# Kernel optimization log

Hardware: AMD Instinct MI355X
Metric: run time of the kernel (lower is better)

## Reference

```python
import jax, jax.numpy as jnp
import numpy as np

N_NODES = 100000
N_EDGES = 1000000
M_DIM = 4
HID = 64
N_GRAPHS = 64


def setup_inputs() -> dict:
    key = jax.random.key(0)
    ks = jax.random.split(key, 16)
    x = jax.random.normal(ks[0], (N_NODES, 1, M_DIM), dtype=jnp.float32)
    edge_index = jax.random.randint(ks[1], (2, N_EDGES), 0, N_NODES, dtype=jnp.int64)
    batch = jnp.sort(jax.random.randint(ks[2], (N_NODES,), 0, N_GRAPHS, dtype=jnp.int64))
    def lin(k, out_c, in_c):
        bound = 1.0 / np.sqrt(in_c)
        return jax.random.uniform(k, (out_c, in_c), jnp.float32, -bound, bound)
    inp = {"x": x, "edge_index": edge_index, "batch": batch}
    inp["W1l"] = lin(ks[3], HID, 1); inp["b1l"] = jnp.zeros((HID,), jnp.float32)
    inp["W1r"] = lin(ks[4], HID, 1)
    inp["W2l"] = lin(ks[5], HID, HID); inp["b2l"] = jnp.zeros((HID,), jnp.float32)
    inp["W2r"] = lin(ks[6], HID, HID)
    inp["W3l"] = lin(ks[7], HID, HID); inp["b3l"] = jnp.zeros((HID,), jnp.float32)
    inp["W3r"] = lin(ks[8], HID, HID)
    inp["Wlin"] = lin(ks[9], 1, HID); inp["blin"] = jnp.zeros((1,), jnp.float32)
    return inp


def _sage_conv(x, src, dst, Wl, bl, Wr):
    # x: [N, F, M]; mean aggregation over in-edges, then lin_l/lin_r GEMMs.
    N, F, M = x.shape
    msg = x[src]  # [E, F, M] gather
    s = jax.ops.segment_sum(msg, dst, num_segments=N)
    cnt = jax.ops.segment_sum(jnp.ones((src.shape[0],), x.dtype), dst, num_segments=N)
    agg = s / jnp.maximum(cnt, 1.0)[:, None, None]  # [N, F, M]
    C = Wl.shape[0]
    # torch .view(N*M, F) on contiguous [N,F,M] == row-major reshape (mixes F and M)
    h = (agg.reshape(N * M, F) @ Wl.T + bl).reshape(N, C, M)
    h = h + (x.reshape(N * M, F) @ Wr.T).reshape(N, C, M)
    return h


def reference(x, edge_index, batch, W1l, b1l, W1r, W2l, b2l, W2r, W3l, b3l, W3r, Wlin, blin):
    src, dst = edge_index[0], edge_index[1]
    h = jax.nn.relu(_sage_conv(x, src, dst, W1l, b1l, W1r))
    h = jax.nn.relu(_sage_conv(h, src, dst, W2l, b2l, W2r))
    h = jax.nn.relu(_sage_conv(h, src, dst, W3l, b3l, W3r))
    # new_global_mean_pool: scatter-mean over nodes -> [B, HID, M]
    sums = jax.ops.segment_sum(h, batch, num_segments=N_GRAPHS)
    cnts = jax.ops.segment_sum(jnp.ones((h.shape[0],), h.dtype), batch, num_segments=N_GRAPHS)
    pooled = sums / jnp.maximum(cnts, 1.0)[:, None, None]
    # dropout in eval mode == identity
    B, F, M = pooled.shape
    z = (pooled.reshape(B * M, F) @ Wlin.T + blin).reshape(B, M)
    return jax.nn.sigmoid(z).mean(axis=1)  # [B]
```

## Files before the change

### kernel.cpp

```cpp
#include <hip/hip_runtime.h>
#include <math.h>

#define TPB 256

typedef unsigned short ushort_t;
typedef unsigned char uchar_t;
typedef __attribute__((ext_vector_type(8))) short short8v;
typedef __attribute__((ext_vector_type(4))) float f32x4;
typedef __attribute__((ext_vector_type(8))) unsigned short ushort8;

__device__ __forceinline__ unsigned short f2b(float f) {
  union { float f; unsigned int i; } c; c.f = f;
  unsigned int x = c.i;
  x += 0x7FFFu + ((x >> 16) & 1u);
  return (unsigned short)(x >> 16);
}

__device__ __forceinline__ short8v fp8x8_to_bf16(const uchar_t* p) {
  uint2 u = *(const uint2*)p;
  auto p0 = __builtin_amdgcn_cvt_pk_f32_fp8(u.x, false);
  auto p1 = __builtin_amdgcn_cvt_pk_f32_fp8(u.x, true);
  auto p2 = __builtin_amdgcn_cvt_pk_f32_fp8(u.y, false);
  auto p3 = __builtin_amdgcn_cvt_pk_f32_fp8(u.y, true);
  ushort8 o;
  o[0] = f2b(p0[0]); o[1] = f2b(p0[1]); o[2] = f2b(p1[0]); o[3] = f2b(p1[1]);
  o[4] = f2b(p2[0]); o[5] = f2b(p2[1]); o[6] = f2b(p3[0]); o[7] = f2b(p3[1]);
  union { ushort8 a; short8v b; } c; c.a = o; return c.b;
}

__global__ void k_histg(const int* __restrict__ dst, int* deg,
                        const int* __restrict__ batch, int* gcnt, int E, int N) {
  int t = blockIdx.x * TPB + threadIdx.x;
  if (t < E) atomicAdd(&deg[dst[t]], 1);
  int n0 = t * 16;
  if (n0 < N) {
    int n1 = min(n0 + 16, N);
    int cur = batch[n0];
    int c = 0;
    for (int n = n0; n < n1; ++n) {
      int b = batch[n];
      if (b != cur) { atomicAdd(&gcnt[cur], c); cur = b; c = 0; }
      ++c;
    }
    atomicAdd(&gcnt[cur], c);
  }
}

__global__ void k_scan1(const int* __restrict__ deg, int* rp, int* bsum, int N) {
  __shared__ int s[TPB];
  int t = threadIdx.x;
  int i = blockIdx.x * TPB + t;
  int v = (i < N) ? ((deg[i] + 7) & ~7) : 0;
  s[t] = v;
  __syncthreads();
  for (int d = 1; d < TPB; d <<= 1) {
    int u = (t >= d) ? s[t - d] : 0;
    __syncthreads();
    s[t] += u;
    __syncthreads();
  }
  if (i < N) rp[i] = s[t] - v;
  if (t == TPB - 1) bsum[blockIdx.x] = s[t];
}

__global__ void k_scan2(const int* bsum, int* boff, int nb) {
  __shared__ int s[1024];
  int t = threadIdx.x;
  int v = (t < nb) ? bsum[t] : 0;
  s[t] = v;
  __syncthreads();
  for (int d = 1; d < 1024; d <<= 1) {
    int u = (t >= d) ? s[t - d] : 0;
    __syncthreads();
    s[t] += u;
    __syncthreads();
  }
  if (t < nb) boff[t] = s[t] - v;
}

__global__ void k_scan3(int* rp, const int* __restrict__ boff, const int* __restrict__ bsum,
                        int* cursor, int N, int nb) {
  int i = blockIdx.x * TPB + threadIdx.x;
  if (i < N) {
    int v = rp[i] + boff[i >> 8];
    rp[i] = v;
    cursor[i] = v;
  } else if (i == N) {
    rp[N] = boff[nb - 1] + bsum[nb - 1];
  }
}

__global__ void k_fill(const int* __restrict__ src, const int* __restrict__ dst,
                       int* cursor, int* __restrict__ csr, int E) {
  int e = blockIdx.x * TPB + threadIdx.x;
  if (e < E) {
    int p = atomicAdd(&cursor[dst[e]], 1);
    csr[p] = src[e];
  }
}

__global__ void k_cvtw(const float* __restrict__ s0, const float* __restrict__ s1,
                       const float* __restrict__ s2, const float* __restrict__ s3,
                       ushort_t* d0, ushort_t* d1, ushort_t* d2, ushort_t* d3,
                       uchar_t* zr0, int n) {
  int i = blockIdx.x * TPB + threadIdx.x;
  if (i < n) { d0[i] = f2b(s0[i]); d1[i] = f2b(s1[i]); d2[i] = f2b(s2[i]); d3[i] = f2b(s3[i]); }
  if (blockIdx.x == 0 && threadIdx.x < 64) ((int*)zr0)[threadIdx.x] = 0;
}

__global__ void k_agg1(const float4* __restrict__ x, const int* __restrict__ rp,
                       const int* __restrict__ deg, const int* __restrict__ cursor,
                       int* __restrict__ csr, float4* __restrict__ agg1, int N) {
  int n = blockIdx.x * TPB + threadIdx.x;
  if (n >= N) return;
  int b = rp[n], e = rp[n + 1];
  float4 a = make_float4(0.f, 0.f, 0.f, 0.f);
  for (int i = b; i < e; i += 8) {
    int4 c0 = *(const int4*)(csr + i);
    int4 c1 = *(const int4*)(csr + i + 4);
    int id[8] = {c0.x, c0.y, c0.z, c0.w, c1.x, c1.y, c1.z, c1.w};
#pragma unroll
    for (int j = 0; j < 8; ++j) {
      unsigned idx = min((unsigned)id[j], (unsigned)(N - 1));
      float m = ((unsigned)id[j] < (unsigned)N) ? 1.f : 0.f;
      float4 v = x[idx];
      a.x += v.x * m; a.y += v.y * m; a.z += v.z * m; a.w += v.w * m;
    }
  }
  int d = deg[n];
  float inv = (d > 0) ? 1.f / (float)d : 0.f;
  a.x *= inv; a.y *= inv; a.z *= inv; a.w *= inv;
  agg1[n] = a;
  int c = cursor[n];
  for (int p2 = c; p2 < e; ++p2) csr[p2] = N;
}

__global__ __launch_bounds__(256) void k_gemm(
    const uchar_t* __restrict__ hIn8,
    const float* __restrict__ xf, const float* __restrict__ agg1f,
    const float* __restrict__ W1l, const float* __restrict__ b1l,
    const float* __restrict__ W1r,
    const ushort_t* __restrict__ Wlb, const ushort_t* __restrict__ Wrb,
    const float* __restrict__ bias,
    uchar_t* __restrict__ Yl8, uchar_t* __restrict__ Yr8, int rows) {
  int t = threadIdx.x;
  int wave = t >> 6, lane = t & 63;
  int g = lane >> 4, l15 = lane & 15;
  int r0 = blockIdx.x * 64 + wave * 16;
  int r = r0 + l15;

  short8v af0, af1;
  if (hIn8) {
    const uchar_t* hrow = hIn8 + (size_t)r * 64;
    af0 = fp8x8_to_bf16(hrow + g * 8);
    af1 = fp8x8_to_bf16(hrow + 32 + g * 8);
  } else {
    float sA = agg1f[r], sX = xf[r];
    ushort8 o0, o1;
#pragma unroll
    for (int k = 0; k < 8; ++k) {
      int c0 = g * 8 + k, c1 = 32 + g * 8 + k;
      o0[k] = f2b(fmaxf(sA * W1l[c0] + b1l[c0] + sX * W1r[c0], 0.f));
      o1[k] = f2b(fmaxf(sA * W1l[c1] + b1l[c1] + sX * W1r[c1], 0.f));
    }
    union { ushort8 a; short8v b; } u0, u1;
    u0.a = o0; u1.a = o1;
    af0 = u0.b; af1 = u1.b;
  }

#pragma unroll
  for (int c = 0; c < 4; ++c) {
    const ushort_t* wl = Wlb + (size_t)(c * 16 + l15) * 64;
    const ushort_t* wr = Wrb + (size_t)(c * 16 + l15) * 64;
    short8v bl0 = *(const short8v*)(wl + g * 8);
    short8v bl1 = *(const short8v*)(wl + 32 + g * 8);
    short8v br0 = *(const short8v*)(wr + g * 8);
    short8v br1 = *(const short8v*)(wr + 32 + g * 8);
    float bv = bias[c * 16 + l15];
    f32x4 accl = (f32x4){0.f, 0.f, 0.f, 0.f};
    f32x4 accr = (f32x4){bv, bv, bv, bv};
    accl = __builtin_amdgcn_mfma_f32_16x16x32_bf16(af0, bl0, accl, 0, 0, 0);
    accl = __builtin_amdgcn_mfma_f32_16x16x32_bf16(af1, bl1, accl, 0, 0, 0);
    accr = __builtin_amdgcn_mfma_f32_16x16x32_bf16(af0, br0, accr, 0, 0, 0);
    accr = __builtin_amdgcn_mfma_f32_16x16x32_bf16(af1, br1, accr, 0, 0, 0);
#pragma unroll
    for (int i = 0; i < 4; ++i) {
      size_t off = (size_t)(r0 + g * 4 + i) * 64 + c * 16 + l15;
      Yl8[off] = (uchar_t)(__builtin_amdgcn_cvt_pk_fp8_f32(accl[i], accl[i], 0u, false) & 0xFF);
      Yr8[off] = (uchar_t)(__builtin_amdgcn_cvt_pk_fp8_f32(accr[i], accr[i], 0u, false) & 0xFF);
    }
  }
}

#define ADD8(IDX) { \
    uint2 v = *(const uint2*)(base + ((size_t)(unsigned)(IDX) << 8)); \
    auto q0 = __builtin_amdgcn_cvt_pk_f32_fp8(v.x, false); \
    auto q1 = __builtin_amdgcn_cvt_pk_f32_fp8(v.x, true);  \
    auto q2 = __builtin_amdgcn_cvt_pk_f32_fp8(v.y, false); \
    auto q3 = __builtin_amdgcn_cvt_pk_f32_fp8(v.y, true);  \
    acc[0] += q0[0]; acc[1] += q0[1]; acc[2] += q1[0]; acc[3] += q1[1]; \
    acc[4] += q2[0]; acc[5] += q2[1]; acc[6] += q3[0]; acc[7] += q3[1]; }

__global__ __launch_bounds__(256) void k_gather(
    const uchar_t* __restrict__ Yl8, const uchar_t* __restrict__ Yr8,
    const int* __restrict__ rp, const int* __restrict__ deg, const int* __restrict__ csr,
    uchar_t* __restrict__ hOut8, int N) {
  int tid = blockIdx.x * TPB + threadIdx.x;
  int n = tid >> 5, s = tid & 31;
  if (n >= N) return;
  int b = rp[n], e = rp[n + 1];
  const uchar_t* base = Yl8 + s * 8;

  float acc[8];
#pragma unroll
  for (int j = 0; j < 8; ++j) acc[j] = 0.f;

  for (int i = b; i < e; i += 8) {
    int4 c0 = *(const int4*)(csr + i);
    int4 c1 = *(const int4*)(csr + i + 4);
    ADD8(c0.x) ADD8(c0.y) ADD8(c0.z) ADD8(c0.w)
    ADD8(c1.x) ADD8(c1.y) ADD8(c1.z) ADD8(c1.w)
  }

  int d = deg[n];
  float inv = (d > 0) ? 1.f / (float)d : 0.f;
  uint2 yr = *(const uint2*)(Yr8 + (size_t)n * 256 + s * 8);
  auto y0 = __builtin_amdgcn_cvt_pk_f32_fp8(yr.x, false);
  auto y1 = __builtin_amdgcn_cvt_pk_f32_fp8(yr.x, true);
  auto y2 = __builtin_amdgcn_cvt_pk_f32_fp8(yr.y, false);
  auto y3 = __builtin_amdgcn_cvt_pk_f32_fp8(yr.y, true);
  float h0 = fmaxf(acc[0] * inv + y0[0], 0.f);
  float h1 = fmaxf(acc[1] * inv + y0[1], 0.f);
  float h2 = fmaxf(acc[2] * inv + y1[0], 0.f);
  float h3 = fmaxf(acc[3] * inv + y1[1], 0.f);
  float h4 = fmaxf(acc[4] * inv + y2[0], 0.f);
  float h5 = fmaxf(acc[5] * inv + y2[1], 0.f);
  float h6 = fmaxf(acc[6] * inv + y3[0], 0.f);
  float h7 = fmaxf(acc[7] * inv + y3[1], 0.f);
  unsigned int w0 = __builtin_amdgcn_cvt_pk_fp8_f32(h0, h1, 0u, false);
  w0 = __builtin_amdgcn_cvt_pk_fp8_f32(h2, h3, w0, true);
  unsigned int w1 = __builtin_amdgcn_cvt_pk_fp8_f32(h4, h5, 0u, false);
  w1 = __builtin_amdgcn_cvt_pk_fp8_f32(h6, h7, w1, true);
  uint2 st; st.x = w0; st.y = w1;
  *(uint2*)(hOut8 + (size_t)n * 256 + s * 8) = st;
}

__device__ __forceinline__ float fp8_to_f32(uchar_t u) {
  return __builtin_amdgcn_cvt_pk_f32_fp8((unsigned int)u, false)[0];
}

__global__ void k_pool(const uchar_t* __restrict__ h, const int* __restrict__ batch,
                       float* pooled, int N) {
  int t = threadIdx.x;
  int nPer = (N + gridDim.x - 1) / gridDim.x;
  int n0 = blockIdx.x * nPer;
  int n1 = min(N, n0 + nPer);
  if (n0 >= n1) return;
  float acc = 0.f;
  int cur = batch[n0];
  int n = n0;
  for (; n + 3 < n1; n += 4) {
    int b0 = batch[n], b3 = batch[n + 3];
    float v0 = fp8_to_f32(h[(size_t)n * 256 + t]);
    float v1 = fp8_to_f32(h[(size_t)(n + 1) * 256 + t]);
    float v2 = fp8_to_f32(h[(size_t)(n + 2) * 256 + t]);
    float v3 = fp8_to_f32(h[(size_t)(n + 3) * 256 + t]);
    if (b0 == b3) {
      if (b0 != cur) { atomicAdd(&pooled[cur * 256 + t], acc); acc = 0.f; cur = b0; }
      acc += (v0 + v1) + (v2 + v3);
    } else {
      int bb1 = batch[n + 1], bb2 = batch[n + 2];
      int bb[4] = {b0, bb1, bb2, b3};
      float vv[4] = {v0, v1, v2, v3};
#pragma unroll
      for (int j = 0; j < 4; ++j) {
        if (bb[j] != cur) { atomicAdd(&pooled[cur * 256 + t], acc); acc = 0.f; cur = bb[j]; }
        acc += vv[j];
      }
    }
  }
  for (; n < n1; ++n) {
    int b = batch[n];
    if (b != cur) { atomicAdd(&pooled[cur * 256 + t], acc); acc = 0.f; cur = b; }
    acc += fp8_to_f32(h[(size_t)n * 256 + t]);
  }
  atomicAdd(&pooled[cur * 256 + t], acc);
}

__global__ void k_final(const float* __restrict__ pooled, const int* __restrict__ gcnt,
                        const float* __restrict__ Wlin, const float* __restrict__ blin,
                        float* __restrict__ out, int B) {
  int t = blockIdx.x * TPB + threadIdx.x;
  int b = t >> 2, j = t & 3;
  if (b >= B) return;
  float inv = 1.f / fmaxf((float)gcnt[b], 1.f);
  float s = blin[0];
  const float* p = pooled + b * 256 + j * 64;
#pragma unroll
  for (int f = 0; f < 64; ++f) s += p[f] * inv * Wlin[f];
  float z = 1.f / (1.f + expf(-s));
  z += __shfl_xor(z, 1);
  z += __shfl_xor(z, 2);
  if (j == 0) out[b] = 0.25f * z;
}

extern "C" void kernel_launch(void* const* d_in, const int* in_sizes, int n_in,
                              void* d_out, int out_size, void* d_ws, size_t ws_size,
                              hipStream_t stream) {
  const float* x   = (const float*)d_in[0];
  const int* edge  = (const int*)d_in[1];
  const int* batch = (const int*)d_in[2];
  const float* W1l = (const float*)d_in[3];
  const float* b1l = (const float*)d_in[4];
  const float* W1r = (const float*)d_in[5];
  const float* W2l = (const float*)d_in[6];
  const float* b2l = (const float*)d_in[7];
  const float* W2r = (const float*)d_in[8];
  const float* W3l = (const float*)d_in[9];
  const float* b3l = (const float*)d_in[10];
  const float* W3r = (const float*)d_in[11];
  const float* Wlin = (const float*)d_in[12];
  const float* blin = (const float*)d_in[13];
  float* out = (float*)d_out;

  const int N = in_sizes[0] / 4;
  const int E = in_sizes[1] / 2;
  const int B = out_size;
  const int rows = 4 * N;

  const int* srcA = edge;
  const int* dstA = edge + E;

  char* p = (char*)d_ws;
  auto carve = [&](size_t bytes) -> void* {
    void* r = (void*)p;
    p += (bytes + 255) & ~(size_t)255;
    return r;
  };
  char* zstart = p;
  int* deg     = (int*)carve((size_t)N * 4);
  int* gcnt    = (int*)carve((size_t)B * 4);
  float* pooled = (float*)carve((size_t)B * 256 * 4);
  size_t zlen  = (size_t)(p - zstart);
  int* rp      = (int*)carve((size_t)(N + 1) * 4);
  int* cursor  = (int*)carve((size_t)N * 4);
  int* bsum    = (int*)carve(4096);
  int* boff    = (int*)carve(4096);
  int* csr     = (int*)carve(((size_t)E + 8 * (size_t)N) * 4);
  float* agg1  = (float*)carve((size_t)N * 4 * 4);
  ushort_t* Wb2l = (ushort_t*)carve(4096 * 2);
  ushort_t* Wb2r = (ushort_t*)carve(4096 * 2);
  ushort_t* Wb3l = (ushort_t*)carve(4096 * 2);
  ushort_t* Wb3r = (ushort_t*)carve(4096 * 2);
  uchar_t* Yl8 = (uchar_t*)carve(((size_t)N + 1) * 256);
  uchar_t* Yr8 = (uchar_t*)carve((size_t)N * 256);
  uchar_t* h8  = (uchar_t*)carve((size_t)N * 256);
  (void)ws_size; (void)n_in;

  hipMemsetAsync(zstart, 0, zlen, stream);

  int nbScan = (N + TPB - 1) / TPB;

  k_histg<<<(E + TPB - 1) / TPB, TPB, 0, stream>>>(dstA, deg, batch, gcnt, E, N);
  k_cvtw<<<16, TPB, 0, stream>>>(W2l, W2r, W3l, W3r, Wb2l, Wb2r, Wb3l, Wb3r,
                                 Yl8 + (size_t)N * 256, 4096);
  k_scan1<<<nbScan, TPB, 0, stream>>>(deg, rp, bsum, N);
  k_scan2<<<1, 1024, 0, stream>>>(bsum, boff, nbScan);
  k_scan3<<<(N + 1 + TPB - 1) / TPB, TPB, 0, stream>>>(rp, boff, bsum, cursor, N, nbScan);
  k_fill<<<(E + TPB - 1) / TPB, TPB, 0, stream>>>(srcA, dstA, cursor, csr, E);

  k_agg1<<<(N + TPB - 1) / TPB, TPB, 0, stream>>>((const float4*)x, rp, deg, cursor,
                                                  csr, (float4*)agg1, N);

  int nbGemm = (rows + 63) / 64;
  int nbGather = ((size_t)N * 32 + TPB - 1) / TPB;

  k_gemm<<<nbGemm, TPB, 0, stream>>>((const uchar_t*)nullptr, x, agg1, W1l, b1l, W1r,
                                     Wb2l, Wb2r, b2l, Yl8, Yr8, rows);
  k_gather<<<nbGather, TPB, 0, stream>>>(Yl8, Yr8, rp, deg, csr, h8, N);

  k_gemm<<<nbGemm, TPB, 0, stream>>>(h8, x, agg1, W1l, b1l, W1r,
                                     Wb3l, Wb3r, b3l, Yl8, Yr8, rows);
  k_gather<<<nbGather, TPB, 0, stream>>>(Yl8, Yr8, rp, deg, csr, h8, N);

  k_pool<<<1024, TPB, 0, stream>>>(h8, batch, pooled, N);
  k_final<<<(B * 4 + TPB - 1) / TPB, TPB, 0, stream>>>(pooled, gcnt, Wlin, blin, out, B);
}
```

Baseline: 393.1 us.

## Bin edges by destination block for CSR fill and fuse pooling into final gather

The CSR fill becomes a two-pass binning. Edges are first scattered into coarse destination-block bins, and then each block places its bin's edges with atomics that stay local to that block, which should improve atomic and write locality. Separately, the last gather kernel now does the global mean-pool directly. It reduces across the block through shared memory when all 8 nodes belong to one graph and falls back to per-element atomics otherwise, so h8 is never written out and the separate pool kernel is gone. The cost is an extra pass over an 8-byte-per-edge bin buffer and more atomics in blocks that straddle a graph boundary.

```diff
diff --git a/kernel.cpp b/kernel.cpp
--- a/kernel.cpp
+++ b/kernel.cpp
@@ -90,12 +90,48 @@
   }
 }
 
-__global__ void k_fill(const int* __restrict__ src, const int* __restrict__ dst,
-                       int* cursor, int* __restrict__ csr, int E) {
+__global__ void k_bscan(const int* __restrict__ deg, int* bbase, int* bcur, int N, int nbk, int bshift) {
+  __shared__ int s[1024];
+  int t = threadIdx.x;
+  int cnt = 0;
+  if (t < nbk) {
+    int n0 = t << bshift, n1 = min(n0 + (1 << bshift), N);
+    for (int n = n0; n < n1; ++n) cnt += deg[n];
+  }
+  s[t] = cnt;
+  __syncthreads();
+  for (int d = 1; d < 1024; d <<= 1) {
+    int u = (t >= d) ? s[t - d] : 0;
+    __syncthreads();
+    s[t] += u;
+    __syncthreads();
+  }
+  if (t < nbk) {
+    int base = s[t] - cnt;
+    bbase[t] = base;
+    bcur[t] = base;
+    if (t == nbk - 1) bbase[nbk] = s[t];
+  }
+}
+
+__global__ void k_binA(const int* __restrict__ src, const int* __restrict__ dst,
+                       int* bcur, int2* __restrict__ binbuf, int E, int bshift) {
   int e = blockIdx.x * TPB + threadIdx.x;
   if (e < E) {
-    int p = atomicAdd(&cursor[dst[e]], 1);
-    csr[p] = src[e];
+    int d = dst[e], s = src[e];
+    int pos = atomicAdd(&bcur[d >> bshift], 1);
+    binbuf[pos] = make_int2(d, s);
+  }
+}
+
+__global__ void k_binB(const int2* __restrict__ binbuf, const int* __restrict__ bbase,
+                       int* cursor, int* __restrict__ csr) {
+  int b = blockIdx.x;
+  int lo = bbase[b], hi = bbase[b + 1];
+  for (int i = lo + threadIdx.x; i < hi; i += TPB) {
+    int2 pr = binbuf[i];
+    int p = atomicAdd(&cursor[pr.x], 1);
+    csr[p] = pr.y;
   }
 }
 
@@ -204,87 +240,85 @@
 __global__ __launch_bounds__(256) void k_gather(
     const uchar_t* __restrict__ Yl8, const uchar_t* __restrict__ Yr8,
     const int* __restrict__ rp, const int* __restrict__ deg, const int* __restrict__ csr,
-    uchar_t* __restrict__ hOut8, int N) {
+    uchar_t* __restrict__ hOut8, float* __restrict__ pooled,
+    const int* __restrict__ batch, int N) {
+  __shared__ float ps[1024];
   int tid = blockIdx.x * TPB + threadIdx.x;
   int n = tid >> 5, s = tid & 31;
-  if (n >= N) return;
-  int b = rp[n], e = rp[n + 1];
-  const uchar_t* base = Yl8 + s * 8;
+  bool alive = (n < N);
 
   float acc[8];
 #pragma unroll
   for (int j = 0; j < 8; ++j) acc[j] = 0.f;
 
-  for (int i = b; i < e; i += 8) {
-    int4 c0 = *(const int4*)(csr + i);
-    int4 c1 = *(const int4*)(csr + i + 4);
-    ADD8(c0.x) ADD8(c0.y) ADD8(c0.z) ADD8(c0.w)
-    ADD8(c1.x) ADD8(c1.y) ADD8(c1.z) ADD8(c1.w)
-  }
-
-  int d = deg[n];
-  float inv = (d > 0) ? 1.f / (float)d : 0.f;
-  uint2 yr = *(const uint2*)(Yr8 + (size_t)n * 256 + s * 8);
-  auto y0 = __builtin_amdgcn_cvt_pk_f32_fp8(yr.x, false);
-  auto y1 = __builtin_amdgcn_cvt_pk_f32_fp8(yr.x, true);
-  auto y2 = __builtin_amdgcn_cvt_pk_f32_fp8(yr.y, false);
-  auto y3 = __builtin_amdgcn_cvt_pk_f32_fp8(yr.y, true);
-  float h0 = fmaxf(acc[0] * inv + y0[0], 0.f);
-  float h1 = fmaxf(acc[1] * inv + y0[1], 0.f);
-  float h2 = fmaxf(acc[2] * inv + y1[0], 0.f);
-  float h3 = fmaxf(acc[3] * inv + y1[1], 0.f);
-  float h4 = fmaxf(acc[4] * inv + y2[0], 0.f);
-  float h5 = fmaxf(acc[5] * inv + y2[1], 0.f);
-  float h6 = fmaxf(acc[6] * inv + y3[0], 0.f);
-  float h7 = fmaxf(acc[7] * inv + y3[1], 0.f);
-  unsigned int w0 = __builtin_amdgcn_cvt_pk_fp8_f32(h0, h1, 0u, false);
-  w0 = __builtin_amdgcn_cvt_pk_fp8_f32(h2, h3, w0, true);
-  unsigned int w1 = __builtin_amdgcn_cvt_pk_fp8_f32(h4, h5, 0u, false);
-  w1 = __builtin_amdgcn_cvt_pk_fp8_f32(h6, h7, w1, true);
-  uint2 st; st.x = w0; st.y = w1;
-  *(uint2*)(hOut8 + (size_t)n * 256 + s * 8) = st;
-}
-
-__device__ __forceinline__ float fp8_to_f32(uchar_t u) {
-  return __builtin_amdgcn_cvt_pk_f32_fp8((unsigned int)u, false)[0];
-}
-
-__global__ void k_pool(const uchar_t* __restrict__ h, const int* __restrict__ batch,
-                       float* pooled, int N) {
-  int t = threadIdx.x;
-  int nPer = (N + gridDim.x - 1) / gridDim.x;
-  int n0 = blockIdx.x * nPer;
-  int n1 = min(N, n0 + nPer);
-  if (n0 >= n1) return;
-  float acc = 0.f;
-  int cur = batch[n0];
-  int n = n0;
-  for (; n + 3 < n1; n += 4) {
-    int b0 = batch[n], b3 = batch[n + 3];
-    float v0 = fp8_to_f32(h[(size_t)n * 256 + t]);
-    float v1 = fp8_to_f32(h[(size_t)(n + 1) * 256 + t]);
-    float v2 = fp8_to_f32(h[(size_t)(n + 2) * 256 + t]);
-    float v3 = fp8_to_f32(h[(size_t)(n + 3) * 256 + t]);
-    if (b0 == b3) {
-      if (b0 != cur) { atomicAdd(&pooled[cur * 256 + t], acc); acc = 0.f; cur = b0; }
-      acc += (v0 + v1) + (v2 + v3);
-    } else {
-      int bb1 = batch[n + 1], bb2 = batch[n + 2];
-      int bb[4] = {b0, bb1, bb2, b3};
-      float vv[4] = {v0, v1, v2, v3};
-#pragma unroll
-      for (int j = 0; j < 4; ++j) {
-        if (bb[j] != cur) { atomicAdd(&pooled[cur * 256 + t], acc); acc = 0.f; cur = bb[j]; }
-        acc += vv[j];
-      }
-    }
-  }
-  for (; n < n1; ++n) {
-    int b = batch[n];
-    if (b != cur) { atomicAdd(&pooled[cur * 256 + t], acc); acc = 0.f; cur = b; }
-    acc += fp8_to_f32(h[(size_t)n * 256 + t]);
-  }
-  atomicAdd(&pooled[cur * 256 + t], acc);
+  float h[8];
+#pragma unroll
+  for (int j = 0; j < 8; ++j) h[j] = 0.f;
+
+  if (alive) {
+    int b = rp[n], e = rp[n + 1];
+    const uchar_t* base = Yl8 + s * 8;
+    for (int i = b; i < e; i += 8) {
+      int4 c0 = *(const int4*)(csr + i);
+      int4 c1 = *(const int4*)(csr + i + 4);
+      ADD8(c0.x) ADD8(c0.y) ADD8(c0.z) ADD8(c0.w)
+      ADD8(c1.x) ADD8(c1.y) ADD8(c1.z) ADD8(c1.w)
+    }
+    int d = deg[n];
+    float inv = (d > 0) ? 1.f / (float)d : 0.f;
+    uint2 yr = *(const uint2*)(Yr8 + (size_t)n * 256 + s * 8);
+    auto y0 = __builtin_amdgcn_cvt_pk_f32_fp8(yr.x, false);
+    auto y1 = __builtin_amdgcn_cvt_pk_f32_fp8(yr.x, true);
+    auto y2 = __builtin_amdgcn_cvt_pk_f32_fp8(yr.y, false);
+    auto y3 = __builtin_amdgcn_cvt_pk_f32_fp8(yr.y, true);
+    h[0] = fmaxf(acc[0] * inv + y0[0], 0.f);
+    h[1] = fmaxf(acc[1] * inv + y0[1], 0.f);
+    h[2] = fmaxf(acc[2] * inv + y1[0], 0.f);
+    h[3] = fmaxf(acc[3] * inv + y1[1], 0.f);
+    h[4] = fmaxf(acc[4] * inv + y2[0], 0.f);
+    h[5] = fmaxf(acc[5] * inv + y2[1], 0.f);
+    h[6] = fmaxf(acc[6] * inv + y3[0], 0.f);
+    h[7] = fmaxf(acc[7] * inv + y3[1], 0.f);
+  }
+
+  if (hOut8) {
+    if (alive) {
+      unsigned int w0 = __builtin_amdgcn_cvt_pk_fp8_f32(h[0], h[1], 0u, false);
+      w0 = __builtin_amdgcn_cvt_pk_fp8_f32(h[2], h[3], w0, true);
+      unsigned int w1 = __builtin_amdgcn_cvt_pk_fp8_f32(h[4], h[5], 0u, false);
+      w1 = __builtin_amdgcn_cvt_pk_fp8_f32(h[6], h[7], w1, true);
+      uint2 st; st.x = w0; st.y = w1;
+      *(uint2*)(hOut8 + (size_t)n * 256 + s * 8) = st;
+    }
+    return;
+  }
+
+  int nb0 = (blockIdx.x * TPB) >> 5;
+  int nlast = min(nb0 + 7, N - 1);
+  int bF = batch[nb0], bL = batch[nlast];
+  if (bF == bL) {
+    int wave = threadIdx.x >> 6;
+    int lane = threadIdx.x & 63;
+#pragma unroll
+    for (int j = 0; j < 8; ++j) h[j] += __shfl_xor(h[j], 32);
+    if (lane < 32) {
+#pragma unroll
+      for (int j = 0; j < 8; ++j) ps[wave * 256 + s * 8 + j] = h[j];
+    }
+    __syncthreads();
+    int t = threadIdx.x;
+    if (t < 256) {
+      float v = ps[t] + ps[256 + t] + ps[512 + t] + ps[768 + t];
+      atomicAdd(&pooled[bF * 256 + t], v);
+    }
+  } else {
+    if (alive) {
+      int bb = batch[n];
+#pragma unroll
+      for (int j = 0; j < 8; ++j)
+        atomicAdd(&pooled[bb * 256 + s * 8 + j], h[j]);
+    }
+  }
 }
 
 __global__ void k_final(const float* __restrict__ pooled, const int* __restrict__ gcnt,
@@ -331,6 +365,10 @@
   const int* srcA = edge;
   const int* dstA = edge + E;
 
+  int bshift = 7;
+  while (((N + (1 << bshift) - 1) >> bshift) > 1024) ++bshift;
+  int nbk = (N + (1 << bshift) - 1) >> bshift;
+
   char* p = (char*)d_ws;
   auto carve = [&](size_t bytes) -> void* {
     void* r = (void*)p;
@@ -346,6 +384,9 @@
   int* cursor  = (int*)carve((size_t)N * 4);
   int* bsum    = (int*)carve(4096);
   int* boff    = (int*)carve(4096);
+  int* bbase   = (int*)carve(4100 * 4);
+  int* bcur    = (int*)carve(4096 * 4);
+  int2* binbuf = (int2*)carve((size_t)E * 8);
   int* csr     = (int*)carve(((size_t)E + 8 * (size_t)N) * 4);
   float* agg1  = (float*)carve((size_t)N * 4 * 4);
   ushort_t* Wb2l = (ushort_t*)carve(4096 * 2);
@@ -367,7 +408,9 @@
   k_scan1<<<nbScan, TPB, 0, stream>>>(deg, rp, bsum, N);
   k_scan2<<<1, 1024, 0, stream>>>(bsum, boff, nbScan);
   k_scan3<<<(N + 1 + TPB - 1) / TPB, TPB, 0, stream>>>(rp, boff, bsum, cursor, N, nbScan);
-  k_fill<<<(E + TPB - 1) / TPB, TPB, 0, stream>>>(srcA, dstA, cursor, csr, E);
+  k_bscan<<<1, 1024, 0, stream>>>(deg, bbase, bcur, N, nbk, bshift);
+  k_binA<<<(E + TPB - 1) / TPB, TPB, 0, stream>>>(srcA, dstA, bcur, binbuf, E, bshift);
+  k_binB<<<nbk, TPB, 0, stream>>>(binbuf, bbase, cursor, csr);
 
   k_agg1<<<(N + TPB - 1) / TPB, TPB, 0, stream>>>((const float4*)x, rp, deg, cursor,
                                                   csr, (float4*)agg1, N);
@@ -377,12 +420,13 @@
 
   k_gemm<<<nbGemm, TPB, 0, stream>>>((const uchar_t*)nullptr, x, agg1, W1l, b1l, W1r,
                                      Wb2l, Wb2r, b2l, Yl8, Yr8, rows);
-  k_gather<<<nbGather, TPB, 0, stream>>>(Yl8, Yr8, rp, deg, csr, h8, N);
+  k_gather<<<nbGather, TPB, 0, stream>>>(Yl8, Yr8, rp, deg, csr, h8,
+                                         (float*)nullptr, batch, N);
 
   k_gemm<<<nbGemm, TPB, 0, stream>>>(h8, x, agg1, W1l, b1l, W1r,
                                      Wb3l, Wb3r, b3l, Yl8, Yr8, rows);
-  k_gather<<<nbGather, TPB, 0, stream>>>(Yl8, Yr8, rp, deg, csr, h8, N);
-
-  k_pool<<<1024, TPB, 0, stream>>>(h8, batch, pooled, N);
+  k_gather<<<nbGather, TPB, 0, stream>>>(Yl8, Yr8, rp, deg, csr, (uchar_t*)nullptr,
+                                         pooled, batch, N);
+
   k_final<<<(B * 4 + TPB - 1) / TPB, TPB, 0, stream>>>(pooled, gcnt, Wlin, blin, out, B);
 }
```

After: 635.5 us. +61.6%, slower.
